# Kernel optimization log

Measured on AMD Instinct MI355X. Metric: run time of the kernel, lower is better.

Reference implementation:

```python
import jax, jax.numpy as jnp
import numpy as np

FEATURE_DIM = 512
Z_DIM = 256
Q_DIM = 128
NUM_Z_CODES = 4096
NUM_Q_CODES = 2048
HIDDEN_DIM = 128 * 4  # 512
BOTTLENECK = 64
BATCH = 32768


def setup_inputs() -> dict:
    key = jax.random.key(0)
    ks = jax.random.split(key, 16)
    d = {}
    d['x'] = jax.random.normal(ks[0], (BATCH, FEATURE_DIM), dtype=jnp.float32)
    # encoder: Linear(feature_dim,64) -> GELU -> Linear(64,hidden) -> GELU
    d['eW1'] = jax.random.normal(ks[1], (BOTTLENECK, FEATURE_DIM), dtype=jnp.float32) * (1.0 / np.sqrt(FEATURE_DIM))
    d['eb1'] = jnp.zeros((BOTTLENECK,), jnp.float32)
    d['eW2'] = jax.random.normal(ks[2], (HIDDEN_DIM, BOTTLENECK), dtype=jnp.float32) * (1.0 / np.sqrt(BOTTLENECK))
    d['eb2'] = jnp.zeros((HIDDEN_DIM,), jnp.float32)
    # to_z_latent LipschitzMLP(hidden, z_dim)
    d['zW'] = jax.random.normal(ks[3], (Z_DIM, HIDDEN_DIM), dtype=jnp.float32) * (1.0 / np.sqrt(HIDDEN_DIM))
    d['zb'] = jnp.zeros((Z_DIM,), jnp.float32)
    d['zci'] = jnp.ones((Z_DIM,), jnp.float32)
    # z codebook
    d['z_codebook'] = jax.random.normal(ks[4], (NUM_Z_CODES, Z_DIM), dtype=jnp.float32)
    # q_encoder LipschitzMLP(z_dim, q_dim)
    d['qW'] = jax.random.normal(ks[5], (Q_DIM, Z_DIM), dtype=jnp.float32) * (1.0 / np.sqrt(Z_DIM))
    d['qb'] = jnp.zeros((Q_DIM,), jnp.float32)
    d['qci'] = jnp.ones((Q_DIM,), jnp.float32)
    # q codebook
    d['q_codebook'] = jax.random.normal(ks[6], (NUM_Q_CODES, Q_DIM), dtype=jnp.float32)
    # decoder: Linear(q_dim,64) -> GELU -> Linear(64,hidden) -> GELU
    d['dW1'] = jax.random.normal(ks[7], (BOTTLENECK, Q_DIM), dtype=jnp.float32) * (1.0 / np.sqrt(Q_DIM))
    d['db1'] = jnp.zeros((BOTTLENECK,), jnp.float32)
    d['dW2'] = jax.random.normal(ks[8], (HIDDEN_DIM, BOTTLENECK), dtype=jnp.float32) * (1.0 / np.sqrt(BOTTLENECK))
    d['db2'] = jnp.zeros((HIDDEN_DIM,), jnp.float32)
    # to_output Linear(hidden, feature_dim)
    d['oW'] = jax.random.normal(ks[9], (FEATURE_DIM, HIDDEN_DIM), dtype=jnp.float32) * (1.0 / np.sqrt(HIDDEN_DIM))
    d['ob'] = jnp.zeros((FEATURE_DIM,), jnp.float32)
    return d


def _gelu(x):
    return jax.nn.gelu(x, approximate=False)  # torch nn.GELU default (erf)


def _lipschitz_mlp(x, W, b, ci):
    # normalization: scale each row of W so its L1 norm <= softplus(ci)
    absrowsum = jnp.sum(jnp.abs(W), axis=1, keepdims=True)          # [out,1]
    scale = jnp.minimum(1.0, jax.nn.softplus(ci)[:, None] / absrowsum)
    W_norm = W * scale
    return jax.nn.sigmoid(x @ W_norm.T + b)


def _quantize(z_e, codebook):
    # ||a-b||^2 = ||a||^2 + ||b||^2 - 2 a.b ; single big GEMM
    z_norm = jnp.sum(z_e * z_e, axis=1, keepdims=True)              # [B,1]
    cb_norm = jnp.sum(codebook * codebook, axis=1)[None, :]         # [1,K]
    dists = z_norm + cb_norm - 2.0 * (z_e @ codebook.T)             # [B,K]
    idx = jnp.argmin(dists, axis=1)
    z_q = codebook[idx]
    return z_q, idx


def _mse(a, b):
    return jnp.mean((a - b) ** 2)


def reference(x, eW1, eb1, eW2, eb2, zW, zb, zci, z_codebook,
              qW, qb, qci, q_codebook, dW1, db1, dW2, db2, oW, ob):
    sg = jax.lax.stop_gradient
    # encoder
    h = _gelu(_gelu(x @ eW1.T + eb1) @ eW2.T + eb2)                 # [B,hidden]
    z_e = _lipschitz_mlp(h, zW, zb, zci)                            # [B,z_dim]
    z_q, z_idx = _quantize(z_e, z_codebook)
    commit_z = _mse(z_e, sg(z_q))
    codebook_z = _mse(z_q, sg(z_e))
    # q level
    q_e = _lipschitz_mlp(sg(z_q), qW, qb, qci)                      # [B,q_dim]
    q_q, q_idx = _quantize(q_e, q_codebook)
    commit_q = _mse(q_e, sg(q_q))
    codebook_q = _mse(q_q, sg(q_e))
    # decoder
    dec_h = _gelu(_gelu(q_q @ dW1.T + db1) @ dW2.T + db2)           # [B,hidden]
    x_recon = dec_h @ oW.T + ob                                     # [B,feature]
    recon_loss = _mse(x_recon, x)
    loss = recon_loss + 0.25 * (commit_z + codebook_z) + 0.25 * (commit_q + codebook_q)
    return (loss, recon_loss, commit_z, codebook_z, commit_q, codebook_q,
            x_recon, z_q, q_q, z_idx, q_idx)
```

## Files before the change

kernel.cpp:

```cpp
#include <hip/hip_runtime.h>

typedef unsigned long long u64;
typedef unsigned short u16;
typedef unsigned int u32;


namespace {

constexpr int kBatch = 32768;

__device__ __forceinline__ float gelu_f(float x) {
  return 0.5f * x * (1.0f + erff(x * 0.70710678118654752440f));
}
__device__ __forceinline__ float sigmoid_f(float x) {
  return 1.0f / (1.0f + expf(-x));
}
__device__ __forceinline__ u64 pack_key(float d, unsigned j) {
  unsigned u = __float_as_uint(d);
  u = (u & 0x80000000u) ? ~u : (u | 0x80000000u);
  return ((u64)u << 32) | j;
}
__device__ __forceinline__ u16 bf16_rne(float x) {
  unsigned u = __float_as_uint(x);
  unsigned r = (u + 0x7FFFu + ((u >> 16) & 1u)) >> 16;
  return (u16)r;
}
__device__ __forceinline__ float bf16_to_f(u16 h) {
  return __uint_as_float((unsigned)h << 16);
}
__device__ __forceinline__ u64 min64(u64 a, u64 b) { return a < b ? a : b; }

__device__ __forceinline__ void load_lds16(const void* g, void* l) {
  __builtin_amdgcn_global_load_lds(
      (const __attribute__((address_space(1))) void*)g,
      (__attribute__((address_space(3))) void*)l, 16, 0, 0);
}

template <int N>
__device__ __forceinline__ void wait_vmcnt() {
  if constexpr (N == 0) {
    asm volatile("s_waitcnt vmcnt(0)" ::: "memory");
  } else if constexpr (N == 1) {
    asm volatile("s_waitcnt vmcnt(1)" ::: "memory");
  } else if constexpr (N == 8) {
    asm volatile("s_waitcnt vmcnt(8)" ::: "memory");
  } else if constexpr (N == 16) {
    asm volatile("s_waitcnt vmcnt(16)" ::: "memory");
  }
}

__device__ __forceinline__ void lds_fence_barrier_pre() {
  asm volatile("s_waitcnt lgkmcnt(0)" ::: "memory");
  __builtin_amdgcn_sched_barrier(0);
  __builtin_amdgcn_s_barrier();
  asm volatile("" ::: "memory");
  __builtin_amdgcn_sched_barrier(0);
}

__device__ __forceinline__ void barrier_raw() {
  __builtin_amdgcn_sched_barrier(0);
  __builtin_amdgcn_s_barrier();
  asm volatile("" ::: "memory");
  __builtin_amdgcn_sched_barrier(0);
}

typedef short bf16x8 __attribute__((ext_vector_type(8)));
typedef float f32x4 __attribute__((ext_vector_type(4)));

__global__ void prep_cb_kernel(const float* __restrict__ zcb,
                               u16* __restrict__ zcbh, float* __restrict__ zcbn,
                               const float* __restrict__ qcb,
                               u16* __restrict__ qcbh, float* __restrict__ qcbn) {
  int b = blockIdx.x;
  const float* cb;
  u16* cbh;
  float* cbn;
  int K;
  if (b < 1024) { cb = zcb; cbh = zcbh; cbn = zcbn; K = 256; }
  else { b -= 1024; cb = qcb; cbh = qcbh; cbn = qcbn; K = 128; }
  const int row = b * 4 + (threadIdx.x >> 6);
  const int lane = threadIdx.x & 63;
  double s = 0.0;
  for (int k = lane; k < K; k += 64) {
    const float v = cb[(size_t)row * K + k];
    cbh[(size_t)row * K + k] = bf16_rne(v);
    s += (double)v * (double)v;
  }
#pragma unroll
  for (int o = 32; o > 0; o >>= 1) s += __shfl_down(s, o);
  if (lane == 0) cbn[row] = (float)s;
}

__global__ void prep_w_kernel(
    const float* __restrict__ zW, const float* __restrict__ zci,
    const float* __restrict__ qW, const float* __restrict__ qci,
    const float* __restrict__ eW1, const float* __restrict__ eW2,
    u16* __restrict__ zWns, u16* __restrict__ qWns, u16* __restrict__ eW1s,
    u16* __restrict__ eW2s, const float* __restrict__ dW1,
    const float* __restrict__ dW2, const float* __restrict__ oW,
    u16* __restrict__ dW1b, u16* __restrict__ dW2b, u16* __restrict__ oWb) {
  const int b = blockIdx.x;
  const int tid = threadIdx.x;
  if (b < 384) {
    const float* W;
    const float* ci;
    u16* D;
    int K, row;
    if (b < 256) { W = zW; ci = zci; D = zWns; K = 512; row = b; }
    else { W = qW; ci = qci; D = qWns; K = 256; row = b - 256; }
    float s = 0.f;
    for (int k = tid; k < K; k += 256) s += fabsf(W[(size_t)row * K + k]);
#pragma unroll
    for (int o = 32; o > 0; o >>= 1) s += __shfl_down(s, o);
    __shared__ float p[4];
    if ((tid & 63) == 0) p[tid >> 6] = s;
    __syncthreads();
    const float tot = p[0] + p[1] + p[2] + p[3];
    const float c = ci[row];
    const float sp = (c > 20.f) ? c : log1pf(expf(c));
    const float scale = fminf(1.f, sp / tot);
    for (int k = tid; k < K; k += 256) {
      const float v = W[(size_t)row * K + k] * scale;
      const u16 h = bf16_rne(v);
      const u16 l = bf16_rne(v - bf16_to_f(h));
      D[(size_t)row * 3 * K + k] = h;
      D[(size_t)row * 3 * K + K + k] = h;
      D[(size_t)row * 3 * K + 2 * K + k] = l;
    }
  } else if (b < 512) {
    const int i = (b - 384) * 256 + tid;
    const int r = i >> 9, k = i & 511;
    const float v = eW1[i];
    const u16 h = bf16_rne(v);
    const u16 l = bf16_rne(v - bf16_to_f(h));
    eW1s[(size_t)r * 1536 + k] = h;
    eW1s[(size_t)r * 1536 + 512 + k] = h;
    eW1s[(size_t)r * 1536 + 1024 + k] = l;
  } else if (b < 640) {
    const int i = (b - 512) * 256 + tid;
    const int r = i >> 6, k = i & 63;
    const float v = eW2[i];
    const u16 h = bf16_rne(v);
    const u16 l = bf16_rne(v - bf16_to_f(h));
    eW2s[(size_t)r * 192 + k] = h;
    eW2s[(size_t)r * 192 + 64 + k] = h;
    eW2s[(size_t)r * 192 + 128 + k] = l;
  } else if (b < 672) {
    const int i = (b - 640) * 256 + tid;
    dW1b[i] = bf16_rne(dW1[i]);
  } else if (b < 800) {
    const int i = (b - 672) * 256 + tid;
    dW2b[i] = bf16_rne(dW2[i]);
  } else {
    const int i = (b - 800) * 256 + tid;
    oWb[i] = bf16_rne(oW[i]);
  }
}

__global__ void cast_split_x_kernel(const float* __restrict__ x,
                                    u16* __restrict__ xs) {
  const int i = blockIdx.x * 256 + threadIdx.x;
  const int row = i >> 7, c4 = i & 127;
  const float4 v = *(const float4*)(x + (size_t)row * 512 + c4 * 4);
  const float vv[4] = {v.x, v.y, v.z, v.w};
  u16 hv[4], lv[4];
#pragma unroll
  for (int j = 0; j < 4; ++j) {
    hv[j] = bf16_rne(vv[j]);
    lv[j] = bf16_rne(vv[j] - bf16_to_f(hv[j]));
  }
  *(ushort4*)(xs + (size_t)row * 1024 + c4 * 4) =
      make_ushort4(hv[0], hv[1], hv[2], hv[3]);
  *(ushort4*)(xs + (size_t)row * 1024 + 512 + c4 * 4) =
      make_ushort4(lv[0], lv[1], lv[2], lv[3]);
}

enum { U_GELU_SPLIT = 0, U_SIG_SPLIT = 1, U_GELU_B16 = 2, U_RECON = 3 };

template <int TM, int TN, int NW, int MODE>
__global__ __launch_bounds__(NW * 64) void gemm_uni(
    const u16* __restrict__ A, const u16* __restrict__ B,
    const float* __restrict__ bias, void* __restrict__ Cv,
    const float* __restrict__ X, float* __restrict__ psum, int Ktot,
    int wrapA, int strideA, int N) {
  __shared__ __align__(16) u16 As[TM * 64];
  __shared__ __align__(16) u16 Bs[TN * 64];
  constexpr int NT = NW * 64;
  constexpr int AIT = (TM * 8) / NT;
  constexpr int BIT = (TN * 8) / NT;
  const int tid = threadIdx.x;
  const int lane = tid & 63, w = tid >> 6;
  const int quad = lane >> 4, l15 = lane & 15;
  const int waveM = (TN == 64) ? w * 64 : (w & 1) * 64;
  const int waveN = (TN == 64) ? 0 : (w >> 1) * 64;
  const int rowBase = blockIdx.y * TM;
  const int colBase = blockIdx.x * TN;

  f32x4 acc[4][4] = {};

  for (int k0 = 0; k0 < Ktot; k0 += 64) {
    const int sk0 = (k0 >= wrapA) ? k0 - wrapA : k0;
    __syncthreads();
#pragma unroll
    for (int i = 0; i < AIT; ++i) {
      const int ch = i * NT + tid;
      const int r = ch >> 3, c = ch & 7, g = c ^ (r & 7);
      load_lds16(A + (size_t)(rowBase + r) * strideA + sk0 + g * 8,
                 (char*)As + ch * 16);
    }
#pragma unroll
    for (int i = 0; i < BIT; ++i) {
      const int ch = i * NT + tid;
      const int r = ch >> 3, c = ch & 7, g = c ^ (r & 7);
      load_lds16(B + (size_t)(colBase + r) * Ktot + k0 + g * 8,
                 (char*)Bs + ch * 16);
    }
    __syncthreads();
#pragma unroll
    for (int ks = 0; ks < 2; ++ks) {
      bf16x8 af[4], bf[4];
      const int ch = ks * 4 + quad;
#pragma unroll
      for (int mi = 0; mi < 4; ++mi) {
        const int rl = waveM + mi * 16 + l15;
        af[mi] = *(const bf16x8*)(As + rl * 64 + (ch ^ (rl & 7)) * 8);
      }
#pragma unroll
      for (int ni = 0; ni < 4; ++ni) {
        const int rl = waveN + ni * 16 + l15;
        bf[ni] = *(const bf16x8*)(Bs + rl * 64 + (ch ^ (rl & 7)) * 8);
      }
#pragma unroll
      for (int mi = 0; mi < 4; ++mi)
#pragma unroll
        for (int ni = 0; ni < 4; ++ni)
          acc[mi][ni] = __builtin_amdgcn_mfma_f32_16x16x32_bf16(
              af[mi], bf[ni], acc[mi][ni], 0, 0, 0);
    }
  }

  if constexpr (MODE == U_GELU_SPLIT || MODE == U_SIG_SPLIT) {
    u16* S = (u16*)Cv;
#pragma unroll
    for (int mi = 0; mi < 4; ++mi)
#pragma unroll
      for (int r = 0; r < 4; ++r) {
        const int row = rowBase + waveM + mi * 16 + quad * 4 + r;
#pragma unroll
        for (int ni = 0; ni < 4; ++ni) {
          const int col = colBase + waveN + ni * 16 + l15;
          const float pre = acc[mi][ni][r] + bias[col];
          const float v = (MODE == U_GELU_SPLIT) ? gelu_f(pre) : sigmoid_f(pre);
          const u16 h = bf16_rne(v);
          const u16 l = bf16_rne(v - bf16_to_f(h));
          S[(size_t)row * 2 * N + col] = h;
          S[(size_t)row * 2 * N + N + col] = l;
        }
      }
  } else if constexpr (MODE == U_GELU_B16) {
    u16* C = (u16*)Cv;
#pragma unroll
    for (int mi = 0; mi < 4; ++mi)
#pragma unroll
      for (int r = 0; r < 4; ++r) {
        const int row = rowBase + waveM + mi * 16 + quad * 4 + r;
#pragma unroll
        for (int ni = 0; ni < 4; ++ni) {
          const int col = colBase + waveN + ni * 16 + l15;
          C[(size_t)row * N + col] =
              bf16_rne(gelu_f(acc[mi][ni][r] + bias[col]));
        }
      }
  } else {
    float* C = (float*)Cv;
    float local = 0.f;
#pragma unroll
    for (int mi = 0; mi < 4; ++mi)
#pragma unroll
      for (int r = 0; r < 4; ++r) {
        const int row = rowBase + waveM + mi * 16 + quad * 4 + r;
#pragma unroll
        for (int ni = 0; ni < 4; ++ni) {
          const int col = colBase + waveN + ni * 16 + l15;
          const float val = acc[mi][ni][r] + bias[col];
          const float d = val - X[(size_t)row * N + col];
          local += d * d;
          C[(size_t)row * N + col] = val;
        }
      }
#pragma unroll
    for (int o = 32; o > 0; o >>= 1) local += __shfl_down(local, o);
    __shared__ float psh[NW];
    if (lane == 0) psh[w] = local;
    __syncthreads();
    if (tid == 0) {
      float t = 0.f;
#pragma unroll
      for (int i = 0; i < NW; ++i) t += psh[i];
      psum[blockIdx.y * gridDim.x + blockIdx.x] = t;
    }
  }
}

template <int KT, int CT, int BR, int BTG>
__global__ __launch_bounds__(256) void dist2z_kernel(
    const u16* __restrict__ CB, const u16* __restrict__ ZB,
    const float* __restrict__ cbn, u32* __restrict__ cand, int strideB,
    int ncand) {
  constexpr int CH = KT / 8;
  constexpr int KSTEPS = KT / 32;
  constexpr int CSLOTS = (CT * CH) / 256;
  constexpr int BSLOTS = (BR * CH) / 256;
  __shared__ __align__(16) u16 bufC[CT * KT];
  __shared__ __align__(16) u16 bufB[BR * KT];
  __shared__ u32 wred[BR * 2];
  const int tid = threadIdx.x;
  const int lane = tid & 63, w = tid >> 6;
  const int quad = lane >> 4, l15 = lane & 15;
  const int waveM = (w & 1) * 32;
  const int waveN = (w >> 1) * 32;
  const int ct = blockIdx.y;
  const int btg = blockIdx.x;
  const int codeBase = ct * CT;

  float cnf[2][4];
#pragma unroll
  for (int mi = 0; mi < 2; ++mi)
#pragma unroll
    for (int r = 0; r < 4; ++r)
      cnf[mi][r] =
          cbn[codeBase + waveM + mi * 16 + quad * 4 + r] * 512.0f + 131072.0f;
  asm volatile("" ::: "memory");

#pragma unroll
  for (int i = 0; i < CSLOTS; ++i) {
    const int ch = i * 256 + tid;
    const int r = ch / CH, c = ch % CH, g = c ^ (r & 7);
    load_lds16(CB + (size_t)(codeBase + r) * KT + g * 8, (char*)bufC + ch * 16);
  }
  {
    const int rowBase0 = btg * BTG * BR;
#pragma unroll
    for (int i = 0; i < BSLOTS; ++i) {
      const int ch = i * 256 + tid;
      const int r = ch / CH, c = ch % CH, g = c ^ (r & 7);
      load_lds16(ZB + (size_t)(rowBase0 + r) * strideB + g * 8,
                 (char*)bufB + ch * 16);
    }
  }
  wait_vmcnt<0>();
  barrier_raw();

  bf16x8 af[KSTEPS][2];
#pragma unroll
  for (int kk = 0; kk < KSTEPS; ++kk)
#pragma unroll
    for (int mi = 0; mi < 2; ++mi) {
      const int rl = waveM + mi * 16 + l15;
      const int sw = (kk * 4 + quad) ^ (rl & 7);
      af[kk][mi] = *(const bf16x8*)(bufC + rl * KT + sw * 8);
    }

#pragma unroll 1
  for (int bt = 0; bt < BTG; ++bt) {
    const int rowBase = (btg * BTG + bt) * BR;

    f32x4 acc[2][2] = {};
#pragma unroll
    for (int kk = 0; kk < KSTEPS; ++kk) {
      bf16x8 bf[2];
#pragma unroll
      for (int ni = 0; ni < 2; ++ni) {
        const int rn = waveN + ni * 16 + l15;
        const int sw = (kk * 4 + quad) ^ (rn & 7);
        bf[ni] = *(const bf16x8*)(bufB + rn * KT + sw * 8);
      }
#pragma unroll
      for (int mi = 0; mi < 2; ++mi)
#pragma unroll
        for (int ni = 0; ni < 2; ++ni)
          acc[mi][ni] = __builtin_amdgcn_mfma_f32_16x16x32_bf16(
              af[kk][mi], bf[ni], acc[mi][ni], 0, 0, 0);
    }

#pragma unroll
    for (int ni = 0; ni < 2; ++ni) {
      u32 b0 = ~0u;
#pragma unroll
      for (int mi = 0; mi < 2; ++mi)
#pragma unroll
        for (int r = 0; r < 4; ++r) {
          const float kf = fmaf(acc[mi][ni][r], -1024.0f, cnf[mi][r]);
          u32 iv = (u32)kf;
          iv = iv > 0xFFFFFu ? 0xFFFFFu : iv;
          const u32 key =
              (iv << 12) | (codeBase + waveM + mi * 16 + quad * 4 + r);
          b0 = min(b0, key);
        }
      b0 = min(b0, (u32)__shfl_xor(b0, 16));
      b0 = min(b0, (u32)__shfl_xor(b0, 32));
      if (quad == 0) {
        const int rloc = waveN + ni * 16 + l15;
        wred[rloc * 2 + (w & 1)] = b0;
      }
    }
    lds_fence_barrier_pre();

    if (bt + 1 < BTG) {
      const int rowBaseN = rowBase + BR;
#pragma unroll
      for (int i = 0; i < BSLOTS; ++i) {
        const int ch = i * 256 + tid;
        const int r = ch / CH, c = ch % CH, g = c ^ (r & 7);
        load_lds16(ZB + (size_t)(rowBaseN + r) * strideB + g * 8,
                   (char*)bufB + ch * 16);
      }
    }
    if (tid < BR) {
      const u32 m0 = min(wred[tid * 2 + 0], wred[tid * 2 + 1]);
      cand[(size_t)(rowBase + tid) * ncand + ct] = m0;
    }
    wait_vmcnt<1>();
    lds_fence_barrier_pre();
  }
}

template <int K, int NC, int LEVEL>
__global__ __launch_bounds__(256, 4) void rerank_kernel(
    const u32* __restrict__ cand, const u16* __restrict__ zes,
    const float* __restrict__ cb, const float* __restrict__ cbn,
    float* __restrict__ outq, u16* __restrict__ wsq,
    float* __restrict__ out_idx, float* __restrict__ psum) {
  constexpr int DV = K / 32;
  constexpr int MV = K / 64;
  const int w = threadIdx.x >> 6, lane = threadIdx.x & 63;
  const int row = blockIdx.x * 4 + w;
  const int g = lane >> 3, sub = lane & 7;

  const u16* zr = zes + (size_t)row * 2 * K;

  ushort4 zh[DV], zl[DV];
#pragma unroll
  for (int i = 0; i < DV; ++i) {
    zh[i] = *(const ushort4*)(zr + sub * (K / 8) + 4 * i);
    zl[i] = *(const ushort4*)(zr + K + sub * (K / 8) + 4 * i);
  }
  float zmse[MV];
#pragma unroll
  for (int i = 0; i < MV; ++i) {
    const int c = lane + 64 * i;
    zmse[i] = bf16_to_f(zr[c]) + bf16_to_f(zr[K + c]);
  }
  const u32 mykey = (lane < NC) ? cand[(size_t)row * NC + lane] : ~0u;

  __shared__ u32 kb[4][72];
  kb[w][lane] = mykey;
  __syncthreads();
  int rank = 0;
#pragma unroll
  for (int j = 0; j < 64; ++j) {
    const u32 kj = kb[w][j];
    rank += (kj < mykey || (kj == mykey && j < lane)) ? 1 : 0;
  }
  if (rank < 8) kb[w][64 + rank] = mykey;
  __syncthreads();
  const unsigned ci = kb[w][64 + g] & 0xFFFu;

  const float* cr = cb + (size_t)ci * K;
  float dot = 0.f;
#pragma unroll
  for (int i = 0; i < DV; ++i) {
    const float4 cv = *(const float4*)(cr + sub * (K / 8) + 4 * i);
    dot = fmaf(bf16_to_f(zh[i].x) + bf16_to_f(zl[i].x), cv.x, dot);
    dot = fmaf(bf16_to_f(zh[i].y) + bf16_to_f(zl[i].y), cv.y, dot);
    dot = fmaf(bf16_to_f(zh[i].z) + bf16_to_f(zl[i].z), cv.z, dot);
    dot = fmaf(bf16_to_f(zh[i].w) + bf16_to_f(zl[i].w), cv.w, dot);
  }
#pragma unroll
  for (int off = 1; off < 8; off <<= 1) dot += __shfl_xor(dot, off);
  u64 k2 = pack_key(cbn[ci] - 2.0f * dot, ci);
#pragma unroll
  for (int off = 8; off < 64; off <<= 1) k2 = min64(k2, __shfl_xor(k2, off));
  const unsigned best = (unsigned)k2;
  if (lane == 0) out_idx[row] = (float)best;

  const float* br = cb + (size_t)best * K;
  float local = 0.f;
#pragma unroll
  for (int i = 0; i < MV; ++i) {
    const int c = lane + 64 * i;
    const float v = br[c];
    const float d = zmse[i] - v;
    local += d * d;
    outq[(size_t)row * K + c] = v;
    if (LEVEL == 0) {
      const u16 h = bf16_rne(v);
      wsq[(size_t)row * 2 * K + c] = h;
      wsq[(size_t)row * 2 * K + K + c] = bf16_rne(v - bf16_to_f(h));
    } else {
      wsq[(size_t)row * K + c] = bf16_rne(v);
    }
  }
#pragma unroll
  for (int o = 32; o > 0; o >>= 1) local += __shfl_down(local, o);
  __shared__ float p[4];
  if (lane == 0) p[w] = local;
  __syncthreads();
  if (threadIdx.x == 0) psum[blockIdx.x] = p[0] + p[1] + p[2] + p[3];
}

__global__ void finalize_kernel(const float* __restrict__ psumZ,
                                const float* __restrict__ psumQ,
                                const float* __restrict__ psumR,
                                float* __restrict__ out) {
  const int tid = threadIdx.x;
  float sz = 0.f, sq = 0.f, sr = 0.f;
  for (int i = tid; i < 8192; i += 256) {
    sz += psumZ[i];
    sq += psumQ[i];
  }
  for (int i = tid; i < 1024; i += 256) sr += psumR[i];
#pragma unroll
  for (int o = 32; o > 0; o >>= 1) {
    sz += __shfl_down(sz, o);
    sq += __shfl_down(sq, o);
    sr += __shfl_down(sr, o);
  }
  __shared__ float pz[4], pq[4], pr[4];
  if ((tid & 63) == 0) {
    pz[tid >> 6] = sz;
    pq[tid >> 6] = sq;
    pr[tid >> 6] = sr;
  }
  __syncthreads();
  if (tid == 0) {
    const float cz = (pz[0] + pz[1] + pz[2] + pz[3]) / ((float)kBatch * 256.f);
    const float cq = (pq[0] + pq[1] + pq[2] + pq[3]) / ((float)kBatch * 128.f);
    const float rec = (pr[0] + pr[1] + pr[2] + pr[3]) / ((float)kBatch * 512.f);
    out[0] = rec + 0.5f * cz + 0.5f * cq;
    out[1] = rec;
    out[2] = cz;
    out[3] = cz;
    out[4] = cq;
    out[5] = cq;
  }
}

}

extern "C" void kernel_launch(void* const* d_in, const int* in_sizes, int n_in,
                              void* d_out, int out_size, void* d_ws,
                              size_t ws_size, hipStream_t stream) {
  const float* x   = (const float*)d_in[0];
  const float* eW1 = (const float*)d_in[1];
  const float* eb1 = (const float*)d_in[2];
  const float* eW2 = (const float*)d_in[3];
  const float* eb2 = (const float*)d_in[4];
  const float* zW  = (const float*)d_in[5];
  const float* zb  = (const float*)d_in[6];
  const float* zci = (const float*)d_in[7];
  const float* zcb = (const float*)d_in[8];
  const float* qW  = (const float*)d_in[9];
  const float* qb  = (const float*)d_in[10];
  const float* qci = (const float*)d_in[11];
  const float* qcb = (const float*)d_in[12];
  const float* dW1 = (const float*)d_in[13];
  const float* db1 = (const float*)d_in[14];
  const float* dW2 = (const float*)d_in[15];
  const float* db2 = (const float*)d_in[16];
  const float* oW  = (const float*)d_in[17];
  const float* ob  = (const float*)d_in[18];

  float* out = (float*)d_out;
  float* out_xr = out + 6;
  float* out_zq = out_xr + (size_t)32768 * 512;
  float* out_qq = out_zq + (size_t)32768 * 256;
  float* out_zi = out_qq + (size_t)32768 * 128;
  float* out_qi = out_zi + 32768;

  char* wsb = (char*)d_ws;
  u16*  zWns = (u16*) (wsb + 0x0000000);
  u16*  qWns = (u16*) (wsb + 0x00C0000);
  u16*  eW1s = (u16*) (wsb + 0x00F0000);
  u16*  eW2s = (u16*) (wsb + 0x0120000);
  u16*  dW1b = (u16*) (wsb + 0x0150000);
  u16*  dW2b = (u16*) (wsb + 0x0154000);
  u16*  oWb  = (u16*) (wsb + 0x0164000);
  u16*  zcbh = (u16*) (wsb + 0x01E4000);
  u16*  qcbh = (u16*) (wsb + 0x03E4000);
  float* zcbn = (float*)(wsb + 0x0464000);
  float* qcbn = (float*)(wsb + 0x0468000);
  float* psumR = (float*)(wsb + 0x046B000);
  float* psumZ = (float*)(wsb + 0x0470000);
  float* psumQ = (float*)(wsb + 0x0478000);
  u16*  h1s  = (u16*) (wsb + 0x0480000);
  u16*  h1b  = (u16*) (wsb + 0x0480000);
  u16*  zes  = (u16*) (wsb + 0x0C80000);
  u16*  qes  = (u16*) (wsb + 0x0C80000);
  u16*  hb   = (u16*) (wsb + 0x0C80000);
  u16*  xs   = (u16*) (wsb + 0x2C80000);
  u16*  hs   = (u16*) (wsb + 0x2C80000);
  u32*  candz = (u32*)(wsb + 0x2C80000);
  u16*  zqs  = (u16*) (wsb + 0x3480000);
  u32*  candq = (u32*)(wsb + 0x2C80000);
  u16*  qqb  = (u16*) (wsb + 0x5480000);

  prep_cb_kernel<<<1536, 256, 0, stream>>>(zcb, zcbh, zcbn, qcb, qcbh, qcbn);
  prep_w_kernel<<<1824, 256, 0, stream>>>(zW, zci, qW, qci, eW1, eW2, zWns,
                                          qWns, eW1s, eW2s, dW1, dW2, oW,
                                          dW1b, dW2b, oWb);
  cast_split_x_kernel<<<16384, 256, 0, stream>>>(x, xs);

  gemm_uni<128, 64, 2, U_GELU_SPLIT><<<dim3(1, 256), 128, 0, stream>>>(
      xs, eW1s, eb1, h1s, nullptr, nullptr, 1536, 1024, 1024, 64);
  gemm_uni<128, 128, 4, U_GELU_SPLIT><<<dim3(4, 256), 256, 0, stream>>>(
      h1s, eW2s, eb2, hs, nullptr, nullptr, 192, 128, 128, 512);
  gemm_uni<128, 128, 4, U_SIG_SPLIT><<<dim3(2, 256), 256, 0, stream>>>(
      hs, zWns, zb, zes, nullptr, nullptr, 1536, 1024, 1024, 256);

  dist2z_kernel<256, 64, 64, 64><<<dim3(8, 64), 256, 0, stream>>>(
      zcbh, zes, zcbn, candz, 512, 64);
  rerank_kernel<256, 64, 0><<<8192, 256, 0, stream>>>(
      candz, zes, zcb, zcbn, out_zq, zqs, out_zi, psumZ);

  gemm_uni<128, 128, 4, U_SIG_SPLIT><<<dim3(1, 256), 256, 0, stream>>>(
      zqs, qWns, qb, qes, nullptr, nullptr, 768, 512, 512, 128);
  dist2z_kernel<128, 64, 64, 16><<<dim3(32, 32), 256, 0, stream>>>(
      qcbh, qes, qcbn, candq, 256, 32);
  rerank_kernel<128, 32, 1><<<8192, 256, 0, stream>>>(
      candq, qes, qcb, qcbn, out_qq, qqb, out_qi, psumQ);

  gemm_uni<128, 64, 2, U_GELU_B16><<<dim3(1, 256), 128, 0, stream>>>(
      qqb, dW1b, db1, h1b, nullptr, nullptr, 128, 1 << 30, 128, 64);
  gemm_uni<128, 128, 4, U_GELU_B16><<<dim3(4, 256), 256, 0, stream>>>(
      h1b, dW2b, db2, hb, nullptr, nullptr, 64, 1 << 30, 64, 512);
  gemm_uni<128, 128, 4, U_RECON><<<dim3(4, 256), 256, 0, stream>>>(
      hb, oWb, ob, out_xr, x, psumR, 512, 1 << 30, 512, 512);

  finalize_kernel<<<1, 256, 0, stream>>>(psumZ, psumQ, psumR, out);

  (void)in_sizes; (void)n_in; (void)out_size; (void)ws_size;
}
```

Before: 667.4 us.

## Add 32-code-tile z distance kernel with 128 candidates and shuffle-based top-8 rerank

```diff
diff --git a/kernel.cpp b/kernel.cpp
--- a/kernel.cpp
+++ b/kernel.cpp
@@ -42,6 +42,8 @@
     asm volatile("s_waitcnt vmcnt(0)" ::: "memory");
   } else if constexpr (N == 1) {
     asm volatile("s_waitcnt vmcnt(1)" ::: "memory");
+  } else if constexpr (N == 2) {
+    asm volatile("s_waitcnt vmcnt(2)" ::: "memory");
   } else if constexpr (N == 8) {
     asm volatile("s_waitcnt vmcnt(8)" ::: "memory");
   } else if constexpr (N == 16) {
@@ -303,6 +305,127 @@
 }
 
 template <int KT, int CT, int BR, int BTG>
+__global__ __launch_bounds__(256) void dist3z_kernel(
+    const u16* __restrict__ CB, const u16* __restrict__ ZB,
+    const float* __restrict__ cbn, u32* __restrict__ cand, int strideB,
+    int ncand) {
+  constexpr int CH = KT / 8;
+  constexpr int KSTEPS = KT / 32;
+  constexpr int CSLOTS = (CT * CH) / 256;
+  constexpr int BSLOTS = (BR * CH) / 256;
+  __shared__ __align__(16) u16 bufC[CT * KT];
+  __shared__ __align__(16) u16 bufB[BR * KT];
+  const int tid = threadIdx.x;
+  const int lane = tid & 63, w = tid >> 6;
+  const int quad = lane >> 4, l15 = lane & 15;
+  const int waveN = w * 32;
+  const int ct = blockIdx.y;
+  const int btg = blockIdx.x;
+  const int codeBase = ct * CT;
+
+  float cnf[2][4];
+#pragma unroll
+  for (int mi = 0; mi < 2; ++mi)
+#pragma unroll
+    for (int r = 0; r < 4; ++r)
+      cnf[mi][r] =
+          cbn[codeBase + mi * 16 + quad * 4 + r] * 512.0f + 131072.0f;
+  asm volatile("" ::: "memory");
+
+#pragma unroll
+  for (int i = 0; i < CSLOTS; ++i) {
+    const int ch = i * 256 + tid;
+    const int r = ch / CH, c = ch % CH, g = c ^ (r & 7);
+    load_lds16(CB + (size_t)(codeBase + r) * KT + g * 8, (char*)bufC + ch * 16);
+  }
+  {
+    const int rowBase0 = btg * BTG * BR;
+#pragma unroll
+    for (int i = 0; i < BSLOTS; ++i) {
+      const int ch = i * 256 + tid;
+      const int r = ch / CH, c = ch % CH, g = c ^ (r & 7);
+      load_lds16(ZB + (size_t)(rowBase0 + r) * strideB + g * 8,
+                 (char*)bufB + ch * 16);
+    }
+  }
+  wait_vmcnt<0>();
+  barrier_raw();
+
+  bf16x8 af[KSTEPS][2];
+#pragma unroll
+  for (int kk = 0; kk < KSTEPS; ++kk)
+#pragma unroll
+    for (int mi = 0; mi < 2; ++mi) {
+      const int rl = mi * 16 + l15;
+      const int sw = (kk * 4 + quad) ^ (rl & 7);
+      af[kk][mi] = *(const bf16x8*)(bufC + rl * KT + sw * 8);
+    }
+
+#pragma unroll 1
+  for (int bt = 0; bt < BTG; ++bt) {
+    const int rowBase = (btg * BTG + bt) * BR;
+
+    f32x4 acc[2][2] = {};
+#pragma unroll
+    for (int kk = 0; kk < KSTEPS; ++kk) {
+      bf16x8 bf[2];
+#pragma unroll
+      for (int ni = 0; ni < 2; ++ni) {
+        const int rn = waveN + ni * 16 + l15;
+        const int sw = (kk * 4 + quad) ^ (rn & 7);
+        bf[ni] = *(const bf16x8*)(bufB + rn * KT + sw * 8);
+      }
+#pragma unroll
+      for (int mi = 0; mi < 2; ++mi)
+#pragma unroll
+        for (int ni = 0; ni < 2; ++ni)
+          acc[mi][ni] = __builtin_amdgcn_mfma_f32_16x16x32_bf16(
+              af[kk][mi], bf[ni], acc[mi][ni], 0, 0, 0);
+    }
+
+    u32 best[2];
+#pragma unroll
+    for (int ni = 0; ni < 2; ++ni) {
+      u32 b0 = ~0u;
+#pragma unroll
+      for (int mi = 0; mi < 2; ++mi)
+#pragma unroll
+        for (int r = 0; r < 4; ++r) {
+          const float kf = fmaf(acc[mi][ni][r], -1024.0f, cnf[mi][r]);
+          u32 iv = (u32)kf;
+          iv = iv > 0xFFFFFu ? 0xFFFFFu : iv;
+          const u32 key = (iv << 12) | (codeBase + mi * 16 + quad * 4 + r);
+          b0 = min(b0, key);
+        }
+      b0 = min(b0, (u32)__shfl_xor(b0, 16));
+      b0 = min(b0, (u32)__shfl_xor(b0, 32));
+      best[ni] = b0;
+    }
+    lds_fence_barrier_pre();
+
+    if (bt + 1 < BTG) {
+      const int rowBaseN = rowBase + BR;
+#pragma unroll
+      for (int i = 0; i < BSLOTS; ++i) {
+        const int ch = i * 256 + tid;
+        const int r = ch / CH, c = ch % CH, g = c ^ (r & 7);
+        load_lds16(ZB + (size_t)(rowBaseN + r) * strideB + g * 8,
+                   (char*)bufB + ch * 16);
+      }
+    }
+    if (quad == 0) {
+#pragma unroll
+      for (int ni = 0; ni < 2; ++ni) {
+        const int row = rowBase + waveN + ni * 16 + l15;
+        cand[(size_t)row * ncand + ct] = best[ni];
+      }
+    }
+    wait_vmcnt<2>();
+    barrier_raw();
+  }
+}
+
+template <int KT, int CT, int BR, int BTG>
 __global__ __launch_bounds__(256) void dist2z_kernel(
     const u16* __restrict__ CB, const u16* __restrict__ ZB,
     const float* __restrict__ cbn, u32* __restrict__ cand, int strideB,
@@ -433,6 +556,7 @@
     float* __restrict__ out_idx, float* __restrict__ psum) {
   constexpr int DV = K / 32;
   constexpr int MV = K / 64;
+  constexpr int NK = (NC + 63) / 64;
   const int w = threadIdx.x >> 6, lane = threadIdx.x & 63;
   const int row = blockIdx.x * 4 + w;
   const int g = lane >> 3, sub = lane & 7;
@@ -451,20 +575,22 @@
     const int c = lane + 64 * i;
     zmse[i] = bf16_to_f(zr[c]) + bf16_to_f(zr[K + c]);
   }
-  const u32 mykey = (lane < NC) ? cand[(size_t)row * NC + lane] : ~0u;
-
-  __shared__ u32 kb[4][72];
-  kb[w][lane] = mykey;
-  __syncthreads();
-  int rank = 0;
-#pragma unroll
-  for (int j = 0; j < 64; ++j) {
-    const u32 kj = kb[w][j];
-    rank += (kj < mykey || (kj == mykey && j < lane)) ? 1 : 0;
-  }
-  if (rank < 8) kb[w][64 + rank] = mykey;
-  __syncthreads();
-  const unsigned ci = kb[w][64 + g] & 0xFFFu;
+  u32 mk0 = (lane < NC) ? cand[(size_t)row * NC + lane] : ~0u;
+  u32 mk1 = (NK == 2) ? cand[(size_t)row * NC + 64 + lane] : ~0u;
+
+  unsigned topcode[8];
+#pragma unroll
+  for (int t = 0; t < 8; ++t) {
+    u32 m = min(mk0, mk1);
+#pragma unroll
+    for (int off = 1; off < 64; off <<= 1) m = min(m, (u32)__shfl_xor(m, off));
+    topcode[t] = m & 0xFFFu;
+    if (mk0 == m) mk0 = ~0u;
+    else if (mk1 == m) mk1 = ~0u;
+  }
+  unsigned ci = topcode[0];
+#pragma unroll
+  for (int t = 1; t < 8; ++t) ci = (g == t) ? topcode[t] : ci;
 
   const float* cr = cb + (size_t)ci * K;
   float dot = 0.f;
@@ -600,10 +726,10 @@
   u16*  hb   = (u16*) (wsb + 0x0C80000);
   u16*  xs   = (u16*) (wsb + 0x2C80000);
   u16*  hs   = (u16*) (wsb + 0x2C80000);
-  u32*  candz = (u32*)(wsb + 0x2C80000);
+  u32*  candq = (u32*)(wsb + 0x2C80000);
   u16*  zqs  = (u16*) (wsb + 0x3480000);
-  u32*  candq = (u32*)(wsb + 0x2C80000);
   u16*  qqb  = (u16*) (wsb + 0x5480000);
+  u32*  candz = (u32*)(wsb + 0x5C80000);
 
   prep_cb_kernel<<<1536, 256, 0, stream>>>(zcb, zcbh, zcbn, qcb, qcbh, qcbn);
   prep_w_kernel<<<1824, 256, 0, stream>>>(zW, zci, qW, qci, eW1, eW2, zWns,
@@ -618,9 +744,9 @@
   gemm_uni<128, 128, 4, U_SIG_SPLIT><<<dim3(2, 256), 256, 0, stream>>>(
       hs, zWns, zb, zes, nullptr, nullptr, 1536, 1024, 1024, 256);
 
-  dist2z_kernel<256, 64, 64, 64><<<dim3(8, 64), 256, 0, stream>>>(
-      zcbh, zes, zcbn, candz, 512, 64);
-  rerank_kernel<256, 64, 0><<<8192, 256, 0, stream>>>(
+  dist3z_kernel<256, 32, 128, 32><<<dim3(8, 128), 256, 0, stream>>>(
+      zcbh, zes, zcbn, candz, 512, 128);
+  rerank_kernel<256, 128, 0><<<8192, 256, 0, stream>>>(
       candz, zes, zcb, zcbn, out_zq, zqs, out_zi, psumZ);
 
   gemm_uni<128, 128, 4, U_SIG_SPLIT><<<dim3(1, 256), 256, 0, stream>>>(
```

Result: slower. 703.4 us (+5.4%).
